# Performance work log

Hardware: AMD Instinct MI355X
Metric: run time of the kernel (lower is better)

## Reference

```python
import jax, jax.numpy as jnp
import numpy as np

B, S, D = 8, 1024, 1024
H = 16
HD = D // H  # 64
FF = 4 * D   # 4096
EPS = 1e-5


def layer_norm(x, g, b):
    mu = jnp.mean(x, axis=-1, keepdims=True)
    var = jnp.mean(jnp.square(x - mu), axis=-1, keepdims=True)
    return (x - mu) * jax.lax.rsqrt(var + EPS) * g + b


def setup_inputs() -> dict:
    key = jax.random.key(0)
    ks = jax.random.split(key, 16)
    s_in = 1.0 / np.sqrt(D)
    s_ff = 1.0 / np.sqrt(FF)
    return {
        "x": jax.random.normal(ks[0], (B, S, D), jnp.float32),
        "ln1_g": jnp.ones((D,), jnp.float32),
        "ln1_b": jnp.zeros((D,), jnp.float32),
        "ln2_g": jnp.ones((D,), jnp.float32),
        "ln2_b": jnp.zeros((D,), jnp.float32),
        # per-head projections stacked on a leading head axis: [H, D, HD]
        "Wq": jax.random.uniform(ks[1], (H, D, HD), jnp.float32, -s_in, s_in),
        "bq": jax.random.uniform(ks[2], (H, HD), jnp.float32, -s_in, s_in),
        "Wk": jax.random.uniform(ks[3], (H, D, HD), jnp.float32, -s_in, s_in),
        "bk": jax.random.uniform(ks[4], (H, HD), jnp.float32, -s_in, s_in),
        "Wv": jax.random.uniform(ks[5], (H, D, HD), jnp.float32, -s_in, s_in),
        "bv": jax.random.uniform(ks[6], (H, HD), jnp.float32, -s_in, s_in),
        "Wo": jax.random.uniform(ks[7], (D, D), jnp.float32, -s_in, s_in),
        "bo": jax.random.uniform(ks[8], (D,), jnp.float32, -s_in, s_in),
        "W1": jax.random.uniform(ks[9], (D, FF), jnp.float32, -s_in, s_in),
        "b1": jax.random.uniform(ks[10], (FF,), jnp.float32, -s_in, s_in),
        "W2": jax.random.uniform(ks[11], (FF, D), jnp.float32, -s_ff, s_ff),
        "b2": jax.random.uniform(ks[12], (D,), jnp.float32, -s_ff, s_ff),
    }


def attention(h, Wq, bq, Wk, bk, Wv, bv, Wo, bo):
    # h: [B,S,D] -> q/k/v: [B,H,S,HD]
    q = jnp.einsum("bsd,hdk->bhsk", h, Wq) + bq[None, :, None, :]
    k = jnp.einsum("bsd,hdk->bhsk", h, Wk) + bk[None, :, None, :]
    v = jnp.einsum("bsd,hdk->bhsk", h, Wv) + bv[None, :, None, :]
    scores = jnp.einsum("bhsk,bhtk->bhst", q, k) / jnp.sqrt(jnp.float32(HD))
    w = jax.nn.softmax(scores, axis=-1)  # [B,H,S,S]
    o = jnp.einsum("bhst,bhtk->bhsk", w, v)
    # concat heads (head order matches torch.cat over per-head outputs)
    o = o.transpose(0, 2, 1, 3).reshape(h.shape[0], h.shape[1], D)
    return o @ Wo + bo


def reference(x, ln1_g, ln1_b, ln2_g, ln2_b, Wq, bq, Wk, bk, Wv, bv, Wo, bo, W1, b1, W2, b2):
    h = layer_norm(x, ln1_g, ln1_b)
    x = x + attention(h, Wq, bq, Wk, bk, Wv, bv, Wo, bo)
    h2 = layer_norm(x, ln2_g, ln2_b)
    ff = jax.nn.gelu(h2 @ W1 + b1, approximate=False) @ W2 + b2  # dropout in eval = identity
    return x + ff
```

## Files before the change

### kernel.cpp

```cpp
#include <hip/hip_runtime.h>
#include <hip/hip_bf16.h>
#include <math.h>

#define DMODEL 1024
#define NH     16
#define HD     64
#define FFDIM  4096
#define SEQ    1024
#define BATCH  8
#define ROWS   (BATCH * SEQ)

typedef __bf16 bf16x8 __attribute__((ext_vector_type(8)));
typedef __bf16 bf16x4 __attribute__((ext_vector_type(4)));
typedef float  f32x4  __attribute__((ext_vector_type(4)));

__device__ __forceinline__ unsigned short f2bf(float f) {
  unsigned int u = __builtin_bit_cast(unsigned int, f);
  u += 0x7fff + ((u >> 16) & 1);
  return (unsigned short)(u >> 16);
}

__device__ __forceinline__ void gload_lds16(const void* g, void* l) {
  __builtin_amdgcn_global_load_lds(
      (const __attribute__((address_space(1))) unsigned int*)g,
      (__attribute__((address_space(3))) unsigned int*)l, 16, 0, 0);
}

__device__ __forceinline__ bf16x8 tr_read8(const unsigned short* p) {
  bf16x4 lo, hi;
  const __attribute__((address_space(3))) unsigned short* p3 =
      (const __attribute__((address_space(3))) unsigned short*)p;
  asm volatile("ds_read_b64_tr_b16 %0, %2\n\t"
               "ds_read_b64_tr_b16 %1, %2 offset:128"
               : "=v"(lo), "=v"(hi)
               : "v"(p3));
  return __builtin_shufflevector(lo, hi, 0, 1, 2, 3, 4, 5, 6, 7);
}

__global__ __launch_bounds__(256) void ln_bf16_kernel(
    const float* __restrict__ x, const float* __restrict__ g,
    const float* __restrict__ bta, unsigned short* __restrict__ out) {
  int row = blockIdx.x;
  int tid = threadIdx.x;
  int wid = tid >> 6, lane = tid & 63;
  const float4 v = ((const float4*)(x + (size_t)row * DMODEL))[tid];
  float s = v.x + v.y + v.z + v.w;
#pragma unroll
  for (int off = 32; off >= 1; off >>= 1) s += __shfl_xor(s, off, 64);
  __shared__ float red[8];
  if (lane == 0) red[wid] = s;
  __syncthreads();
  float mu = (red[0] + red[1] + red[2] + red[3]) * (1.0f / DMODEL);
  float4 d;
  d.x = v.x - mu; d.y = v.y - mu; d.z = v.z - mu; d.w = v.w - mu;
  float sq = d.x * d.x + d.y * d.y + d.z * d.z + d.w * d.w;
#pragma unroll
  for (int off = 32; off >= 1; off >>= 1) sq += __shfl_xor(sq, off, 64);
  if (lane == 0) red[4 + wid] = sq;
  __syncthreads();
  float var = (red[4] + red[5] + red[6] + red[7]) * (1.0f / DMODEL);
  float rs = rsqrtf(var + 1e-5f);
  const float4 gg = ((const float4*)g)[tid];
  const float4 bb = ((const float4*)bta)[tid];
  ushort4 o;
  o.x = f2bf(d.x * rs * gg.x + bb.x);
  o.y = f2bf(d.y * rs * gg.y + bb.y);
  o.z = f2bf(d.z * rs * gg.z + bb.z);
  o.w = f2bf(d.w * rs * gg.w + bb.w);
  ((ushort4*)(out + (size_t)row * DMODEL))[tid] = o;
}

__global__ __launch_bounds__(256) void transpose_f2b_kernel(
    const float* __restrict__ in, unsigned short* __restrict__ out,
    int R, int C, long long ibs, long long obs) {
  __shared__ float tile[64][65];
  int b = blockIdx.z;
  int r0 = blockIdx.y * 64, c0 = blockIdx.x * 64;
  const float* ip = in + (size_t)b * ibs;
  unsigned short* op = out + (size_t)b * obs;
  int tid = threadIdx.x;
  int rl = tid >> 4, cl = (tid & 15) * 4;
#pragma unroll
  for (int it = 0; it < 4; ++it) {
    int r = it * 16 + rl;
    float4 v = *(const float4*)(ip + (size_t)(r0 + r) * C + c0 + cl);
    tile[r][cl] = v.x; tile[r][cl + 1] = v.y;
    tile[r][cl + 2] = v.z; tile[r][cl + 3] = v.w;
  }
  __syncthreads();
#pragma unroll
  for (int it = 0; it < 4; ++it) {
    int c = it * 16 + rl;
    ushort4 o;
    o.x = f2bf(tile[cl + 0][c]); o.y = f2bf(tile[cl + 1][c]);
    o.z = f2bf(tile[cl + 2][c]); o.w = f2bf(tile[cl + 3][c]);
    *(ushort4*)(op + (size_t)(c0 + c) * R + r0 + cl) = o;
  }
}

__global__ __launch_bounds__(256) void transpose_v_kernel(
    const unsigned short* __restrict__ V, unsigned short* __restrict__ Vt) {
  __shared__ unsigned short tile[64][68];
  int bh = blockIdx.y;
  int b = bh >> 4, h = bh & 15;
  int t0 = blockIdx.x * 64;
  int tid = threadIdx.x;
  int rl = tid >> 4, cl = (tid & 15) * 4;
  const unsigned short* ip = V + ((size_t)(b * SEQ + t0)) * DMODEL + h * HD;
#pragma unroll
  for (int it = 0; it < 4; ++it) {
    int t = it * 16 + rl;
    ushort4 v = *(const ushort4*)(ip + (size_t)t * DMODEL + cl);
    tile[t][cl] = v.x; tile[t][cl + 1] = v.y;
    tile[t][cl + 2] = v.z; tile[t][cl + 3] = v.w;
  }
  __syncthreads();
  unsigned short* op = Vt + ((size_t)bh * HD) * SEQ + t0;
#pragma unroll
  for (int it = 0; it < 4; ++it) {
    int d = it * 16 + rl;
    ushort4 o;
    o.x = tile[cl + 0][d]; o.y = tile[cl + 1][d];
    o.z = tile[cl + 2][d]; o.w = tile[cl + 3][d];
    *(ushort4*)(op + (size_t)d * SEQ + cl) = o;
  }
}

#define QSCALE 0.18033688f
template <int EPI>
__global__ __launch_bounds__(256, 2) void gemm_kernel(
    const unsigned short* __restrict__ A, const unsigned short* __restrict__ Bt,
    const float* __restrict__ bias, const float* __restrict__ resid,
    unsigned short* __restrict__ outb, float* __restrict__ outf,
    int M, int N, int K) {
  __shared__ __align__(16) unsigned short As[128 * 32];
  __shared__ __align__(16) unsigned short Bs[128 * 32];
  int tid = threadIdx.x;
  int wid = tid >> 6, lane = tid & 63;
  int wr = (wid >> 1) * 64, wc = (wid & 1) * 64;
  int by = blockIdx.y * 128, bx = blockIdx.x * 128;
  int l15 = lane & 15, l4 = lane >> 4;
  const f32x4 fz = {0.f, 0.f, 0.f, 0.f};
  f32x4 acc[4][4];
#pragma unroll
  for (int i = 0; i < 4; ++i)
#pragma unroll
    for (int j = 0; j < 4; ++j) acc[i][j] = fz;

  int srow = tid >> 2;
  int schunk = tid & 3;

  for (int k0 = 0; k0 < K; k0 += 32) {
    __syncthreads();
#pragma unroll
    for (int p = 0; p < 2; ++p) {
      int row = p * 64 + srow;
      int g = schunk ^ ((row >> 1) & 3);
      gload_lds16(A + (size_t)(by + row) * K + k0 + g * 8,
                  (char*)As + p * 4096 + tid * 16);
      gload_lds16(Bt + (size_t)(bx + row) * K + k0 + g * 8,
                  (char*)Bs + p * 4096 + tid * 16);
    }
    __syncthreads();
    bf16x8 af[4], bfr[4];
#pragma unroll
    for (int m = 0; m < 4; ++m) {
      int row = wr + m * 16 + l15;
      int phys = l4 ^ ((row >> 1) & 3);
      af[m] = *(const bf16x8*)((const char*)As + row * 64 + phys * 16);
    }
#pragma unroll
    for (int n = 0; n < 4; ++n) {
      int row = wc + n * 16 + l15;
      int phys = l4 ^ ((row >> 1) & 3);
      bfr[n] = *(const bf16x8*)((const char*)Bs + row * 64 + phys * 16);
    }
#pragma unroll
    for (int m = 0; m < 4; ++m)
#pragma unroll
      for (int n = 0; n < 4; ++n)
        acc[m][n] = __builtin_amdgcn_mfma_f32_16x16x32_bf16(af[m], bfr[n],
                                                            acc[m][n], 0, 0, 0);
  }
#pragma unroll
  for (int m = 0; m < 4; ++m) {
#pragma unroll
    for (int n = 0; n < 4; ++n) {
      int col = bx + wc + n * 16 + l15;
      float bn = bias[col];
#pragma unroll
      for (int j = 0; j < 4; ++j) {
        int row = by + wr + m * 16 + l4 * 4 + j;
        float v = acc[m][n][j] + bn;
        if (EPI == 0) {
          outb[(size_t)row * N + col] = f2bf(v);
        } else if (EPI == 1) {
          outf[(size_t)row * N + col] = v + resid[(size_t)row * N + col];
        } else if (EPI == 2) {
          float gel = 0.5f * v * (1.0f + erff(v * 0.70710678118f));
          outb[(size_t)row * N + col] = f2bf(gel);
        } else if (EPI == 3) {
          outf[(size_t)row * N + col] = v + resid[(size_t)row * N + col];
        } else {
          outb[(size_t)row * N + col] = f2bf(v * QSCALE);
        }
      }
    }
  }
}

__global__ __launch_bounds__(256, 3) void attn_kernel(
    const unsigned short* __restrict__ Q, const unsigned short* __restrict__ K,
    const unsigned short* __restrict__ Vt, unsigned short* __restrict__ O) {
  __shared__ __align__(16) unsigned short Ks[128 * 64];
  __shared__ __align__(16) unsigned short Vs[64 * 128];
  __shared__ __align__(16) unsigned short Ps[4][128 * 16];
  int tid = threadIdx.x, wid = tid >> 6, lane = tid & 63;
  int l15 = lane & 15, l4 = lane >> 4;
  int sid = blockIdx.x;
  int aid = (sid & 7) * 256 + (sid >> 3);
  int bh = aid >> 4, qb = aid & 15;
  int b = bh >> 4, h = bh & 15;
  int q0 = qb * 64 + wid * 16;
  const f32x4 fz = {0.f, 0.f, 0.f, 0.f};

  const unsigned short* Qbase = Q + ((size_t)(b * SEQ + q0)) * DMODEL + h * HD;
  bf16x8 qf[2];
#pragma unroll
  for (int kh = 0; kh < 2; ++kh)
    qf[kh] = *(const bf16x8*)(Qbase + (size_t)l15 * DMODEL + kh * 32 + l4 * 8);

  f32x4 o[4];
#pragma unroll
  for (int i = 0; i < 4; ++i) o[i] = fz;
  float mrun[4], lrun[4];
#pragma unroll
  for (int j = 0; j < 4; ++j) { mrun[j] = -1e30f; lrun[j] = 0.0f; }

  const unsigned short* Kb = K + (size_t)b * SEQ * DMODEL + h * HD;
  const unsigned short* Vb = Vt + (size_t)bh * HD * SEQ;
  unsigned short* pbase = &Ps[wid][0];
  int krow = tid >> 3, kchunk = tid & 7;
  int vrow = tid >> 4, vchunk = tid & 15;

  for (int t0 = 0; t0 < SEQ; t0 += 128) {
    __syncthreads();
#pragma unroll
    for (int p = 0; p < 4; ++p) {
      int kr = p * 32 + krow;
      int kg = kchunk ^ (kr & 7);
      gload_lds16(Kb + (size_t)(t0 + kr) * DMODEL + kg * 8,
                  (char*)Ks + p * 4096 + tid * 16);
      int vr = p * 16 + vrow;
      int vg = vchunk ^ (vr & 7);
      gload_lds16(Vb + (size_t)vr * SEQ + t0 + vg * 8,
                  (char*)Vs + p * 4096 + tid * 16);
    }
    __syncthreads();
    f32x4 s[8];
#pragma unroll
    for (int ts = 0; ts < 8; ++ts) {
      int row = ts * 16 + l15;
      bf16x8 k0f = *(const bf16x8*)((const char*)Ks + row * 128 + ((l4) ^ (row & 7)) * 16);
      bf16x8 k1f = *(const bf16x8*)((const char*)Ks + row * 128 + ((4 + l4) ^ (row & 7)) * 16);
      s[ts] = __builtin_amdgcn_mfma_f32_16x16x32_bf16(qf[0], k0f, fz, 0, 0, 0);
      s[ts] = __builtin_amdgcn_mfma_f32_16x16x32_bf16(qf[1], k1f, s[ts], 0, 0, 0);
    }
#pragma unroll
    for (int j = 0; j < 4; ++j) {
      float tm = fmaxf(fmaxf(fmaxf(s[0][j], s[1][j]), fmaxf(s[2][j], s[3][j])),
                       fmaxf(fmaxf(s[4][j], s[5][j]), fmaxf(s[6][j], s[7][j])));
#pragma unroll
      for (int off = 8; off >= 1; off >>= 1) tm = fmaxf(tm, __shfl_xor(tm, off, 16));
      float mnew = fmaxf(mrun[j], tm);
      float alpha = __builtin_amdgcn_exp2f(mrun[j] - mnew);
      float ps = 0.0f;
#pragma unroll
      for (int ts = 0; ts < 8; ++ts) {
        float p = __builtin_amdgcn_exp2f(s[ts][j] - mnew);
        s[ts][j] = p;
        ps += p;
      }
#pragma unroll
      for (int off = 8; off >= 1; off >>= 1) ps += __shfl_xor(ps, off, 16);
      lrun[j] = lrun[j] * alpha + ps;
      mrun[j] = mnew;
#pragma unroll
      for (int d = 0; d < 4; ++d) o[d][j] *= alpha;
    }
#pragma unroll
    for (int ts = 0; ts < 8; ++ts) {
      ushort4 pk;
      pk.x = f2bf(s[ts][0]); pk.y = f2bf(s[ts][1]);
      pk.z = f2bf(s[ts][2]); pk.w = f2bf(s[ts][3]);
      *(ushort4*)((char*)pbase + (ts * 16 + l15) * 32 + l4 * 8) = pk;
    }
    asm volatile("s_waitcnt lgkmcnt(0)" ::: "memory");
    __builtin_amdgcn_sched_barrier(0);
#pragma unroll
    for (int kp = 0; kp < 4; ++kp) {
      bf16x8 pf = tr_read8(pbase + (kp * 32 + l4 * 8) * 16 + l15);
      asm volatile("s_waitcnt lgkmcnt(0)" ::: "memory");
      __builtin_amdgcn_sched_barrier(0);
#pragma unroll
      for (int d = 0; d < 4; ++d) {
        int vr = d * 16 + l15;
        int vphys = (kp * 4 + l4) ^ (vr & 7);
        bf16x8 vf = *(const bf16x8*)((const char*)Vs + vr * 256 + vphys * 16);
        o[d] = __builtin_amdgcn_mfma_f32_16x16x32_bf16(pf, vf, o[d], 0, 0, 0);
      }
    }
  }
  unsigned short* Ob = O + ((size_t)(b * SEQ + q0)) * DMODEL + h * HD;
#pragma unroll
  for (int j = 0; j < 4; ++j) {
    float inv = 1.0f / lrun[j];
#pragma unroll
    for (int d = 0; d < 4; ++d) {
      int row = l4 * 4 + j;
      Ob[(size_t)row * DMODEL + d * 16 + l15] = f2bf(o[d][j] * inv);
    }
  }
}

extern "C" void kernel_launch(void* const* d_in, const int* in_sizes, int n_in,
                              void* d_out, int out_size, void* d_ws, size_t ws_size,
                              hipStream_t stream) {
  (void)in_sizes; (void)n_in; (void)out_size; (void)ws_size;
  const float* x    = (const float*)d_in[0];
  const float* ln1g = (const float*)d_in[1];
  const float* ln1b = (const float*)d_in[2];
  const float* ln2g = (const float*)d_in[3];
  const float* ln2b = (const float*)d_in[4];
  const float* Wq   = (const float*)d_in[5];
  const float* bq   = (const float*)d_in[6];
  const float* Wk   = (const float*)d_in[7];
  const float* bk   = (const float*)d_in[8];
  const float* Wv   = (const float*)d_in[9];
  const float* bv   = (const float*)d_in[10];
  const float* Wo   = (const float*)d_in[11];
  const float* bo   = (const float*)d_in[12];
  const float* W1   = (const float*)d_in[13];
  const float* b1   = (const float*)d_in[14];
  const float* W2   = (const float*)d_in[15];
  const float* b2   = (const float*)d_in[16];
  float* out = (float*)d_out;

  char* ws = (char*)d_ws;
  const size_t MB = 1u << 20;
  unsigned short* wqT = (unsigned short*)(ws + 0 * MB);
  unsigned short* wkT = (unsigned short*)(ws + 2 * MB);
  unsigned short* wvT = (unsigned short*)(ws + 4 * MB);
  unsigned short* woT = (unsigned short*)(ws + 6 * MB);
  unsigned short* w1T = (unsigned short*)(ws + 8 * MB);
  unsigned short* w2T = (unsigned short*)(ws + 16 * MB);
  unsigned short* hb  = (unsigned short*)(ws + 24 * MB);
  unsigned short* Qb  = (unsigned short*)(ws + 40 * MB);
  unsigned short* Kb  = (unsigned short*)(ws + 56 * MB);
  unsigned short* Vb  = (unsigned short*)(ws + 72 * MB);
  unsigned short* Vt  = (unsigned short*)(ws + 88 * MB);
  unsigned short* Ob  = Vb;
  unsigned short* ff1 = (unsigned short*)(ws + 40 * MB);

  transpose_f2b_kernel<<<dim3(1, 16, 16), 256, 0, stream>>>(Wq, wqT, 1024, 64,
                                                            65536LL, 65536LL);
  transpose_f2b_kernel<<<dim3(1, 16, 16), 256, 0, stream>>>(Wk, wkT, 1024, 64,
                                                            65536LL, 65536LL);
  transpose_f2b_kernel<<<dim3(1, 16, 16), 256, 0, stream>>>(Wv, wvT, 1024, 64,
                                                            65536LL, 65536LL);
  transpose_f2b_kernel<<<dim3(16, 16, 1), 256, 0, stream>>>(Wo, woT, 1024, 1024, 0, 0);
  transpose_f2b_kernel<<<dim3(64, 16, 1), 256, 0, stream>>>(W1, w1T, 1024, 4096, 0, 0);
  transpose_f2b_kernel<<<dim3(16, 64, 1), 256, 0, stream>>>(W2, w2T, 4096, 1024, 0, 0);

  ln_bf16_kernel<<<dim3(ROWS), 256, 0, stream>>>(x, ln1g, ln1b, hb);

  gemm_kernel<4><<<dim3(8, 64), 256, 0, stream>>>(hb, wqT, bq, nullptr, Qb, nullptr,
                                                  ROWS, DMODEL, DMODEL);
  gemm_kernel<0><<<dim3(8, 64), 256, 0, stream>>>(hb, wkT, bk, nullptr, Kb, nullptr,
                                                  ROWS, DMODEL, DMODEL);
  gemm_kernel<0><<<dim3(8, 64), 256, 0, stream>>>(hb, wvT, bv, nullptr, Vb, nullptr,
                                                  ROWS, DMODEL, DMODEL);

  transpose_v_kernel<<<dim3(16, 128), 256, 0, stream>>>(Vb, Vt);

  attn_kernel<<<dim3(2048), 256, 0, stream>>>(Qb, Kb, Vt, Ob);

  gemm_kernel<1><<<dim3(8, 64), 256, 0, stream>>>(Ob, woT, bo, x, nullptr, out,
                                                  ROWS, DMODEL, DMODEL);

  ln_bf16_kernel<<<dim3(ROWS), 256, 0, stream>>>(out, ln2g, ln2b, hb);

  gemm_kernel<2><<<dim3(32, 64), 256, 0, stream>>>(hb, w1T, b1, nullptr, ff1, nullptr,
                                                   ROWS, FFDIM, DMODEL);

  gemm_kernel<3><<<dim3(8, 64), 256, 0, stream>>>(ff1, w2T, b2, out, nullptr, out,
                                                  ROWS, DMODEL, FFDIM);
}
```

Baseline: 449.3 us.

## Replace GEMM with 8-wave double-buffered pipelined kernel and larger tiles

```diff
diff --git a/kernel.cpp b/kernel.cpp
--- a/kernel.cpp
+++ b/kernel.cpp
@@ -35,6 +35,21 @@
                : "=v"(lo), "=v"(hi)
                : "v"(p3));
   return __builtin_shufflevector(lo, hi, 0, 1, 2, 3, 4, 5, 6, 7);
+}
+
+template <int N>
+__device__ __forceinline__ void wait_vm_lgkm() {
+  if constexpr (N == 0)
+    asm volatile("s_waitcnt vmcnt(0) lgkmcnt(0)" ::: "memory");
+  else if constexpr (N == 2)
+    asm volatile("s_waitcnt vmcnt(2) lgkmcnt(0)" ::: "memory");
+  else
+    asm volatile("s_waitcnt vmcnt(4) lgkmcnt(0)" ::: "memory");
+  __builtin_amdgcn_sched_barrier(0);
+}
+__device__ __forceinline__ void wait_lgkm() {
+  asm volatile("s_waitcnt lgkmcnt(0)" ::: "memory");
+  __builtin_amdgcn_sched_barrier(0);
 }
 
 __global__ __launch_bounds__(256) void ln_bf16_kernel(
@@ -127,86 +142,200 @@
 }
 
 #define QSCALE 0.18033688f
-template <int EPI>
-__global__ __launch_bounds__(256, 2) void gemm_kernel(
+
+template <int BN, int EPI>
+__global__ __launch_bounds__(512, 2) void gemm8_kernel(
     const unsigned short* __restrict__ A, const unsigned short* __restrict__ Bt,
     const float* __restrict__ bias, const float* __restrict__ resid,
     unsigned short* __restrict__ outb, float* __restrict__ outf,
-    int M, int N, int K) {
-  __shared__ __align__(16) unsigned short As[128 * 32];
-  __shared__ __align__(16) unsigned short Bs[128 * 32];
-  int tid = threadIdx.x;
-  int wid = tid >> 6, lane = tid & 63;
-  int wr = (wid >> 1) * 64, wc = (wid & 1) * 64;
-  int by = blockIdx.y * 128, bx = blockIdx.x * 128;
-  int l15 = lane & 15, l4 = lane >> 4;
+    int M, int N, int K, int NX) {
+  constexpr int WAVE_N = BN / 4;
+  constexpr int NREP = BN / 64;
+  constexpr int BSZB = BN * 128;
+  constexpr int VMN = (BN == 256) ? 4 : 2;
+  __shared__ __align__(16) unsigned short As[2 * 256 * 64];
+  __shared__ __align__(16) unsigned short Bs[2 * BN * 64];
+
+  const int tid = threadIdx.x;
+  const int wid = tid >> 6, lane = tid & 63;
+  const int l15 = lane & 15, l4 = lane >> 4;
+  const int wm = wid >> 2, wn = wid & 3;
+
+  const int cpx = (int)gridDim.x >> 3;
+  const int swz = ((int)blockIdx.x & 7) * cpx + ((int)blockIdx.x >> 3);
+  const int by = swz / NX, bx = swz % NX;
+
+  const size_t KBY = (size_t)K * 2;
+
+  const int rlA0 = wid * 16 + (lane >> 3);
+  const int rlA1 = rlA0 + 8;
+  const char* gA0 = (const char*)A + (size_t)(by * 256 + rlA0) * KBY +
+                    (((lane & 7) ^ (rlA0 & 7)) << 4);
+  const char* gA1 = (const char*)A + (size_t)(by * 256 + rlA1) * KBY +
+                    (((lane & 7) ^ (rlA1 & 7)) << 4);
+  char* ldsA0 = (char*)As + wid * 2048 + lane * 16;
+  char* ldsA1 = ldsA0 + 1024;
+
+  const int rlB0 = (BN == 256) ? (wid * 16 + (lane >> 3)) : (wid * 8 + (lane >> 3));
+  const int rlB1 = rlB0 + 8;
+  const char* gB0 = (const char*)Bt + (size_t)(bx * BN + rlB0) * KBY +
+                    (((lane & 7) ^ (rlB0 & 7)) << 4);
+  const char* gB1 = (const char*)Bt + (size_t)(bx * BN + rlB1) * KBY +
+                    (((lane & 7) ^ (rlB1 & 7)) << 4);
+  char* ldsB0 = (char*)Bs + ((BN == 256) ? (wid * 2048) : (wid * 1024)) + lane * 16;
+  char* ldsB1 = ldsB0 + 1024;
+
+  const char* aRd0 = (const char*)As + (wm * 128 + l15) * 128 + ((l4 ^ (l15 & 7)) << 4);
+  const char* aRd1 = (const char*)As + (wm * 128 + l15) * 128 + (((4 + l4) ^ (l15 & 7)) << 4);
+  const char* bRd0 = (const char*)Bs + (wn * WAVE_N + l15) * 128 + ((l4 ^ (l15 & 7)) << 4);
+  const char* bRd1 = (const char*)Bs + (wn * WAVE_N + l15) * 128 + (((4 + l4) ^ (l15 & 7)) << 4);
+
+  f32x4 acc[8][NREP];
   const f32x4 fz = {0.f, 0.f, 0.f, 0.f};
-  f32x4 acc[4][4];
-#pragma unroll
-  for (int i = 0; i < 4; ++i)
-#pragma unroll
-    for (int j = 0; j < 4; ++j) acc[i][j] = fz;
-
-  int srow = tid >> 2;
-  int schunk = tid & 3;
-
-  for (int k0 = 0; k0 < K; k0 += 32) {
-    __syncthreads();
-#pragma unroll
-    for (int p = 0; p < 2; ++p) {
-      int row = p * 64 + srow;
-      int g = schunk ^ ((row >> 1) & 3);
-      gload_lds16(A + (size_t)(by + row) * K + k0 + g * 8,
-                  (char*)As + p * 4096 + tid * 16);
-      gload_lds16(Bt + (size_t)(bx + row) * K + k0 + g * 8,
-                  (char*)Bs + p * 4096 + tid * 16);
-    }
-    __syncthreads();
-    bf16x8 af[4], bfr[4];
-#pragma unroll
-    for (int m = 0; m < 4; ++m) {
-      int row = wr + m * 16 + l15;
-      int phys = l4 ^ ((row >> 1) & 3);
-      af[m] = *(const bf16x8*)((const char*)As + row * 64 + phys * 16);
-    }
-#pragma unroll
-    for (int n = 0; n < 4; ++n) {
-      int row = wc + n * 16 + l15;
-      int phys = l4 ^ ((row >> 1) & 3);
-      bfr[n] = *(const bf16x8*)((const char*)Bs + row * 64 + phys * 16);
-    }
-#pragma unroll
-    for (int m = 0; m < 4; ++m)
-#pragma unroll
-      for (int n = 0; n < 4; ++n)
-        acc[m][n] = __builtin_amdgcn_mfma_f32_16x16x32_bf16(af[m], bfr[n],
-                                                            acc[m][n], 0, 0, 0);
-  }
-#pragma unroll
-  for (int m = 0; m < 4; ++m) {
-#pragma unroll
-    for (int n = 0; n < 4; ++n) {
-      int col = bx + wc + n * 16 + l15;
+#pragma unroll
+  for (int i = 0; i < 8; ++i)
+#pragma unroll
+    for (int n = 0; n < NREP; ++n) acc[i][n] = fz;
+  bf16x8 af[2][2];
+  bf16x8 baf[NREP][2];
+
+#define STAGE_A(buf, h, kt)                                                    \
+  do {                                                                         \
+    gload_lds16(gA0 + (size_t)(h) * 128 * KBY + (size_t)(kt) * 128,            \
+                ldsA0 + (buf) * 32768 + (h) * 16384);                          \
+    gload_lds16(gA1 + (size_t)(h) * 128 * KBY + (size_t)(kt) * 128,            \
+                ldsA1 + (buf) * 32768 + (h) * 16384);                          \
+  } while (0)
+
+#define STAGE_B(buf, h, kt)                                                    \
+  do {                                                                         \
+    if constexpr (BN == 256) {                                                 \
+      gload_lds16(gB0 + (size_t)(h) * 128 * KBY + (size_t)(kt) * 128,          \
+                  ldsB0 + (buf) * BSZB + (h) * 16384);                         \
+      gload_lds16(gB1 + (size_t)(h) * 128 * KBY + (size_t)(kt) * 128,          \
+                  ldsB1 + (buf) * BSZB + (h) * 16384);                         \
+    } else {                                                                   \
+      gload_lds16(gB0 + (size_t)(h) * 64 * KBY + (size_t)(kt) * 128,           \
+                  ldsB0 + (buf) * BSZB + (h) * 8192);                          \
+    }                                                                          \
+  } while (0)
+
+#define READ_B(buf)                                                            \
+  do {                                                                         \
+    _Pragma("unroll") for (int ni = 0; ni < NREP; ++ni) {                      \
+      baf[ni][0] = *(const bf16x8*)(bRd0 + (buf) * BSZB + ni * 2048);          \
+      baf[ni][1] = *(const bf16x8*)(bRd1 + (buf) * BSZB + ni * 2048);          \
+    }                                                                          \
+  } while (0)
+
+#define READ_A(buf, q)                                                         \
+  do {                                                                         \
+    _Pragma("unroll") for (int m01 = 0; m01 < 2; ++m01) {                      \
+      af[m01][0] = *(const bf16x8*)(aRd0 + (buf) * 32768 + (q) * 4096 + m01 * 2048); \
+      af[m01][1] = *(const bf16x8*)(aRd1 + (buf) * 32768 + (q) * 4096 + m01 * 2048); \
+    }                                                                          \
+  } while (0)
+
+#define MFMA_Q(q)                                                              \
+  do {                                                                         \
+    __builtin_amdgcn_s_setprio(1);                                             \
+    _Pragma("unroll") for (int m01 = 0; m01 < 2; ++m01)                        \
+        _Pragma("unroll") for (int ni = 0; ni < NREP; ++ni)                    \
+            _Pragma("unroll") for (int kk = 0; kk < 2; ++kk)                   \
+                acc[(q) * 2 + m01][ni] =                                       \
+        __builtin_amdgcn_mfma_f32_16x16x32_bf16(af[m01][kk], baf[ni][kk],      \
+                                                acc[(q) * 2 + m01][ni], 0, 0, 0); \
+    __builtin_amdgcn_s_setprio(0);                                             \
+  } while (0)
+
+#define BAR __builtin_amdgcn_s_barrier()
+
+#define ITER(t0, LAST)                                                         \
+  do {                                                                         \
+                                                                      \
+    READ_B(0); READ_A(0, 0);                                                   \
+    STAGE_A(1, 0, (t0) + 1);                                                   \
+    BAR; wait_lgkm(); MFMA_Q(0); BAR;                                          \
+                                                                      \
+    READ_A(0, 1);                                                              \
+    STAGE_A(1, 1, (t0) + 1);                                                   \
+    if (!(LAST)) STAGE_B(0, 0, (t0) + 2);                                      \
+    BAR; wait_lgkm(); MFMA_Q(1); BAR;                                          \
+                                                                      \
+    READ_A(0, 2);                                                              \
+    if (!(LAST)) STAGE_B(0, 1, (t0) + 2);                                      \
+    BAR; wait_lgkm(); MFMA_Q(2); BAR;                                          \
+                                                                      \
+    READ_A(0, 3);                                                              \
+    BAR;                                                                       \
+    if (LAST) wait_vm_lgkm<0>(); else wait_vm_lgkm<VMN>();                     \
+    MFMA_Q(3); BAR;                                                            \
+                                                                      \
+    READ_B(1); READ_A(1, 0);                                                   \
+    if (!(LAST)) STAGE_A(0, 0, (t0) + 2);                                      \
+    BAR; wait_lgkm(); MFMA_Q(0); BAR;                                          \
+                                                                      \
+    READ_A(1, 1);                                                              \
+    if (!(LAST)) STAGE_A(0, 1, (t0) + 2);                                      \
+    BAR; wait_lgkm(); MFMA_Q(1); BAR;                                          \
+                                                                      \
+    READ_A(1, 2);                                                              \
+    if (!(LAST)) STAGE_B(1, 0, (t0) + 3);                                      \
+    BAR; wait_lgkm(); MFMA_Q(2); BAR;                                          \
+                                                                      \
+    READ_A(1, 3);                                                              \
+    if (!(LAST)) STAGE_B(1, 1, (t0) + 3);                                      \
+    BAR;                                                                       \
+    if (LAST) wait_lgkm(); else wait_vm_lgkm<VMN>();                           \
+    MFMA_Q(3); BAR;                                                            \
+  } while (0)
+
+  const int nt = K >> 6;
+  const int J = (nt >> 1) - 1;
+
+  STAGE_A(0, 0, 0);
+  STAGE_A(0, 1, 0);
+  STAGE_B(0, 0, 0);
+  STAGE_B(0, 1, 0);
+  STAGE_B(1, 0, 1);
+  STAGE_B(1, 1, 1);
+  wait_vm_lgkm<VMN>();
+  BAR;
+
+#pragma unroll 1
+  for (int j = 0; j < J; ++j) ITER(2 * j, 0);
+  ITER(2 * J, 1);
+
+#pragma unroll
+  for (int mi = 0; mi < 8; ++mi) {
+#pragma unroll
+    for (int ni = 0; ni < NREP; ++ni) {
+      int col = bx * BN + wn * WAVE_N + ni * 16 + l15;
       float bn = bias[col];
 #pragma unroll
-      for (int j = 0; j < 4; ++j) {
-        int row = by + wr + m * 16 + l4 * 4 + j;
-        float v = acc[m][n][j] + bn;
+      for (int jj = 0; jj < 4; ++jj) {
+        int row = by * 256 + wm * 128 + mi * 16 + l4 * 4 + jj;
+        float v = acc[mi][ni][jj] + bn;
         if (EPI == 0) {
           outb[(size_t)row * N + col] = f2bf(v);
-        } else if (EPI == 1) {
+        } else if (EPI == 1 || EPI == 3) {
           outf[(size_t)row * N + col] = v + resid[(size_t)row * N + col];
         } else if (EPI == 2) {
           float gel = 0.5f * v * (1.0f + erff(v * 0.70710678118f));
           outb[(size_t)row * N + col] = f2bf(gel);
-        } else if (EPI == 3) {
-          outf[(size_t)row * N + col] = v + resid[(size_t)row * N + col];
         } else {
           outb[(size_t)row * N + col] = f2bf(v * QSCALE);
         }
       }
     }
   }
+#undef STAGE_A
+#undef STAGE_B
+#undef READ_A
+#undef READ_B
+#undef MFMA_Q
+#undef BAR
+#undef ITER
 }
 
 __global__ __launch_bounds__(256, 3) void attn_kernel(
@@ -374,25 +503,25 @@
 
   ln_bf16_kernel<<<dim3(ROWS), 256, 0, stream>>>(x, ln1g, ln1b, hb);
 
-  gemm_kernel<4><<<dim3(8, 64), 256, 0, stream>>>(hb, wqT, bq, nullptr, Qb, nullptr,
-                                                  ROWS, DMODEL, DMODEL);
-  gemm_kernel<0><<<dim3(8, 64), 256, 0, stream>>>(hb, wkT, bk, nullptr, Kb, nullptr,
-                                                  ROWS, DMODEL, DMODEL);
-  gemm_kernel<0><<<dim3(8, 64), 256, 0, stream>>>(hb, wvT, bv, nullptr, Vb, nullptr,
-                                                  ROWS, DMODEL, DMODEL);
+  gemm8_kernel<128, 4><<<dim3(256), 512, 0, stream>>>(hb, wqT, bq, nullptr, Qb,
+                                                      nullptr, ROWS, DMODEL, DMODEL, 8);
+  gemm8_kernel<128, 0><<<dim3(256), 512, 0, stream>>>(hb, wkT, bk, nullptr, Kb,
+                                                      nullptr, ROWS, DMODEL, DMODEL, 8);
+  gemm8_kernel<128, 0><<<dim3(256), 512, 0, stream>>>(hb, wvT, bv, nullptr, Vb,
+                                                      nullptr, ROWS, DMODEL, DMODEL, 8);
 
   transpose_v_kernel<<<dim3(16, 128), 256, 0, stream>>>(Vb, Vt);
 
   attn_kernel<<<dim3(2048), 256, 0, stream>>>(Qb, Kb, Vt, Ob);
 
-  gemm_kernel<1><<<dim3(8, 64), 256, 0, stream>>>(Ob, woT, bo, x, nullptr, out,
-                                                  ROWS, DMODEL, DMODEL);
+  gemm8_kernel<128, 1><<<dim3(256), 512, 0, stream>>>(Ob, woT, bo, x, nullptr, out,
+                                                      ROWS, DMODEL, DMODEL, 8);
 
   ln_bf16_kernel<<<dim3(ROWS), 256, 0, stream>>>(out, ln2g, ln2b, hb);
 
-  gemm_kernel<2><<<dim3(32, 64), 256, 0, stream>>>(hb, w1T, b1, nullptr, ff1, nullptr,
-                                                   ROWS, FFDIM, DMODEL);
-
-  gemm_kernel<3><<<dim3(8, 64), 256, 0, stream>>>(ff1, w2T, b2, out, nullptr, out,
-                                                  ROWS, DMODEL, FFDIM);
-}
+  gemm8_kernel<256, 2><<<dim3(512), 512, 0, stream>>>(hb, w1T, b1, nullptr, ff1,
+                                                      nullptr, ROWS, FFDIM, DMODEL, 16);
+
+  gemm8_kernel<128, 3><<<dim3(256), 512, 0, stream>>>(ff1, w2T, b2, out, nullptr, out,
+                                                      ROWS, DMODEL, FFDIM, 8);
+}
```

Result: faster. 411.1 us (-8.5%).

## Double-buffer GEMM with BK=64, 512-thread blocks, XCD swizzle, fused QKV launch

Applied to the files above, without the earlier changes.

```diff
diff --git a/kernel.cpp b/kernel.cpp
--- a/kernel.cpp
+++ b/kernel.cpp
@@ -127,82 +127,133 @@
 }
 
 #define QSCALE 0.18033688f
+
 template <int EPI>
-__global__ __launch_bounds__(256, 2) void gemm_kernel(
+__global__ __launch_bounds__(512, 4) void gemmdb_kernel(
     const unsigned short* __restrict__ A, const unsigned short* __restrict__ Bt,
-    const float* __restrict__ bias, const float* __restrict__ resid,
-    unsigned short* __restrict__ outb, float* __restrict__ outf,
-    int M, int N, int K) {
-  __shared__ __align__(16) unsigned short As[128 * 32];
-  __shared__ __align__(16) unsigned short Bs[128 * 32];
-  int tid = threadIdx.x;
-  int wid = tid >> 6, lane = tid & 63;
-  int wr = (wid >> 1) * 64, wc = (wid & 1) * 64;
-  int by = blockIdx.y * 128, bx = blockIdx.x * 128;
-  int l15 = lane & 15, l4 = lane >> 4;
+    const float* __restrict__ bias, const float* __restrict__ bias2,
+    const float* __restrict__ bias3, const float* __restrict__ resid,
+    unsigned short* __restrict__ outb, unsigned short* __restrict__ outb2,
+    unsigned short* __restrict__ outb3, float* __restrict__ outf,
+    int M, int N, int K, int NX) {
+  __shared__ __align__(16) unsigned short As[2 * 128 * 64];
+  __shared__ __align__(16) unsigned short Bs[2 * 128 * 64];
+
+  const int tid = threadIdx.x;
+  const int wid = tid >> 6, lane = tid & 63;
+  const int l15 = lane & 15, l4 = lane >> 4;
+  const int wm = wid >> 1, wn = wid & 1;
+
+  const int cpx = (int)gridDim.x >> 3;
+  const int swz = ((int)blockIdx.x & 7) * cpx + ((int)blockIdx.x >> 3);
+  const int by = swz / NX, bx = swz % NX;
+
+  const size_t KBY = (size_t)K * 2;
+
+  const int rS = tid >> 3;
+  const int cS = ((tid & 7) ^ (rS & 7)) << 4;
+  const char* gA = (const char*)A + (size_t)(by * 128 + rS) * KBY + cS;
+  const char* gB = (const char*)Bt + (size_t)(bx * 128 + rS) * KBY + cS;
+  char* sA = (char*)As + tid * 16;
+  char* sB = (char*)Bs + tid * 16;
+
+  const int rsw = (l4 ^ (l15 & 7)) << 4;
+  const char* aRd0 = (const char*)As + (wm * 32 + l15) * 128 + rsw;
+  const char* aRd1 = (const char*)As + (wm * 32 + l15) * 128 + (rsw ^ 64);
+  const char* bRd0 = (const char*)Bs + (wn * 64 + l15) * 128 + rsw;
+  const char* bRd1 = (const char*)Bs + (wn * 64 + l15) * 128 + (rsw ^ 64);
+
+  f32x4 acc[2][4];
   const f32x4 fz = {0.f, 0.f, 0.f, 0.f};
-  f32x4 acc[4][4];
-#pragma unroll
-  for (int i = 0; i < 4; ++i)
+#pragma unroll
+  for (int i = 0; i < 2; ++i)
 #pragma unroll
     for (int j = 0; j < 4; ++j) acc[i][j] = fz;
 
-  int srow = tid >> 2;
-  int schunk = tid & 3;
-
-  for (int k0 = 0; k0 < K; k0 += 32) {
-    __syncthreads();
-#pragma unroll
-    for (int p = 0; p < 2; ++p) {
-      int row = p * 64 + srow;
-      int g = schunk ^ ((row >> 1) & 3);
-      gload_lds16(A + (size_t)(by + row) * K + k0 + g * 8,
-                  (char*)As + p * 4096 + tid * 16);
-      gload_lds16(Bt + (size_t)(bx + row) * K + k0 + g * 8,
-                  (char*)Bs + p * 4096 + tid * 16);
-    }
-    __syncthreads();
-    bf16x8 af[4], bfr[4];
-#pragma unroll
-    for (int m = 0; m < 4; ++m) {
-      int row = wr + m * 16 + l15;
-      int phys = l4 ^ ((row >> 1) & 3);
-      af[m] = *(const bf16x8*)((const char*)As + row * 64 + phys * 16);
-    }
-#pragma unroll
-    for (int n = 0; n < 4; ++n) {
-      int row = wc + n * 16 + l15;
-      int phys = l4 ^ ((row >> 1) & 3);
-      bfr[n] = *(const bf16x8*)((const char*)Bs + row * 64 + phys * 16);
-    }
-#pragma unroll
-    for (int m = 0; m < 4; ++m)
-#pragma unroll
-      for (int n = 0; n < 4; ++n)
-        acc[m][n] = __builtin_amdgcn_mfma_f32_16x16x32_bf16(af[m], bfr[n],
-                                                            acc[m][n], 0, 0, 0);
-  }
-#pragma unroll
-  for (int m = 0; m < 4; ++m) {
-#pragma unroll
-    for (int n = 0; n < 4; ++n) {
-      int col = bx + wc + n * 16 + l15;
-      float bn = bias[col];
-#pragma unroll
-      for (int j = 0; j < 4; ++j) {
-        int row = by + wr + m * 16 + l4 * 4 + j;
-        float v = acc[m][n][j] + bn;
-        if (EPI == 0) {
-          outb[(size_t)row * N + col] = f2bf(v);
-        } else if (EPI == 1) {
-          outf[(size_t)row * N + col] = v + resid[(size_t)row * N + col];
-        } else if (EPI == 2) {
-          float gel = 0.5f * v * (1.0f + erff(v * 0.70710678118f));
-          outb[(size_t)row * N + col] = f2bf(gel);
-        } else if (EPI == 3) {
-          outf[(size_t)row * N + col] = v + resid[(size_t)row * N + col];
-        } else {
-          outb[(size_t)row * N + col] = f2bf(v * QSCALE);
+  const int nt = K >> 6;
+
+  gload_lds16(gA, sA);
+  gload_lds16(gA + 64 * KBY, sA + 8192);
+  gload_lds16(gB, sB);
+  gload_lds16(gB + 64 * KBY, sB + 8192);
+  asm volatile("s_waitcnt vmcnt(0)" ::: "memory");
+  __builtin_amdgcn_sched_barrier(0);
+  __builtin_amdgcn_s_barrier();
+  __builtin_amdgcn_sched_barrier(0);
+
+#pragma unroll 1
+  for (int t = 0; t < nt; ++t) {
+    const int cur = t & 1;
+    if (t + 1 < nt) {
+      const size_t ko = (size_t)(t + 1) << 7;
+      const int nb = (cur ^ 1) << 14;
+      gload_lds16(gA + ko, sA + nb);
+      gload_lds16(gA + 64 * KBY + ko, sA + nb + 8192);
+      gload_lds16(gB + ko, sB + nb);
+      gload_lds16(gB + 64 * KBY + ko, sB + nb + 8192);
+    }
+    const int off = cur << 14;
+#pragma unroll
+    for (int kk = 0; kk < 2; ++kk) {
+      const char* aR = (kk ? aRd1 : aRd0) + off;
+      const char* bR = (kk ? bRd1 : bRd0) + off;
+      bf16x8 afr[2], bfr[4];
+#pragma unroll
+      for (int ni = 0; ni < 4; ++ni) bfr[ni] = *(const bf16x8*)(bR + ni * 2048);
+#pragma unroll
+      for (int mi = 0; mi < 2; ++mi) afr[mi] = *(const bf16x8*)(aR + mi * 2048);
+      __builtin_amdgcn_s_setprio(1);
+#pragma unroll
+      for (int mi = 0; mi < 2; ++mi)
+#pragma unroll
+        for (int ni = 0; ni < 4; ++ni)
+          acc[mi][ni] = __builtin_amdgcn_mfma_f32_16x16x32_bf16(
+              afr[mi], bfr[ni], acc[mi][ni], 0, 0, 0);
+      __builtin_amdgcn_s_setprio(0);
+    }
+    asm volatile("s_waitcnt vmcnt(0)" ::: "memory");
+    __builtin_amdgcn_sched_barrier(0);
+    __builtin_amdgcn_s_barrier();
+    __builtin_amdgcn_sched_barrier(0);
+  }
+
+  if (EPI == 5) {
+    const int range = bx >> 3;
+    const float* bp = (range == 0) ? bias : (range == 1) ? bias2 : bias3;
+    unsigned short* op = (range == 0) ? outb : (range == 1) ? outb2 : outb3;
+    const float scale = (range == 0) ? QSCALE : 1.0f;
+#pragma unroll
+    for (int mi = 0; mi < 2; ++mi) {
+#pragma unroll
+      for (int ni = 0; ni < 4; ++ni) {
+        int colL = (bx & 7) * 128 + wn * 64 + ni * 16 + l15;
+        float bn = bp[colL];
+#pragma unroll
+        for (int jj = 0; jj < 4; ++jj) {
+          int row = by * 128 + wm * 32 + mi * 16 + l4 * 4 + jj;
+          op[(size_t)row * 1024 + colL] = f2bf((acc[mi][ni][jj] + bn) * scale);
+        }
+      }
+    }
+  } else {
+#pragma unroll
+    for (int mi = 0; mi < 2; ++mi) {
+#pragma unroll
+      for (int ni = 0; ni < 4; ++ni) {
+        int col = bx * 128 + wn * 64 + ni * 16 + l15;
+        float bn = bias[col];
+#pragma unroll
+        for (int jj = 0; jj < 4; ++jj) {
+          int row = by * 128 + wm * 32 + mi * 16 + l4 * 4 + jj;
+          float v = acc[mi][ni][jj] + bn;
+          if (EPI == 1 || EPI == 3) {
+            outf[(size_t)row * N + col] = v + resid[(size_t)row * N + col];
+          } else if (EPI == 2) {
+            float gel = 0.5f * v * (1.0f + erff(v * 0.70710678118f));
+            outb[(size_t)row * N + col] = f2bf(gel);
+          } else {
+            outb[(size_t)row * N + col] = f2bf(v);
+          }
         }
       }
     }
@@ -374,25 +425,24 @@
 
   ln_bf16_kernel<<<dim3(ROWS), 256, 0, stream>>>(x, ln1g, ln1b, hb);
 
-  gemm_kernel<4><<<dim3(8, 64), 256, 0, stream>>>(hb, wqT, bq, nullptr, Qb, nullptr,
-                                                  ROWS, DMODEL, DMODEL);
-  gemm_kernel<0><<<dim3(8, 64), 256, 0, stream>>>(hb, wkT, bk, nullptr, Kb, nullptr,
-                                                  ROWS, DMODEL, DMODEL);
-  gemm_kernel<0><<<dim3(8, 64), 256, 0, stream>>>(hb, wvT, bv, nullptr, Vb, nullptr,
-                                                  ROWS, DMODEL, DMODEL);
+  gemmdb_kernel<5><<<dim3(1536), 512, 0, stream>>>(
+      hb, wqT, bq, bk, bv, nullptr, Qb, Kb, Vb, nullptr, ROWS, 1024, DMODEL, 24);
 
   transpose_v_kernel<<<dim3(16, 128), 256, 0, stream>>>(Vb, Vt);
 
   attn_kernel<<<dim3(2048), 256, 0, stream>>>(Qb, Kb, Vt, Ob);
 
-  gemm_kernel<1><<<dim3(8, 64), 256, 0, stream>>>(Ob, woT, bo, x, nullptr, out,
-                                                  ROWS, DMODEL, DMODEL);
+  gemmdb_kernel<1><<<dim3(512), 512, 0, stream>>>(
+      Ob, woT, bo, nullptr, nullptr, x, nullptr, nullptr, nullptr, out,
+      ROWS, DMODEL, DMODEL, 8);
 
   ln_bf16_kernel<<<dim3(ROWS), 256, 0, stream>>>(out, ln2g, ln2b, hb);
 
-  gemm_kernel<2><<<dim3(32, 64), 256, 0, stream>>>(hb, w1T, b1, nullptr, ff1, nullptr,
-                                                   ROWS, FFDIM, DMODEL);
-
-  gemm_kernel<3><<<dim3(8, 64), 256, 0, stream>>>(ff1, w2T, b2, out, nullptr, out,
-                                                  ROWS, DMODEL, FFDIM);
-}
+  gemmdb_kernel<2><<<dim3(2048), 512, 0, stream>>>(
+      hb, w1T, b1, nullptr, nullptr, nullptr, ff1, nullptr, nullptr, nullptr,
+      ROWS, FFDIM, DMODEL, 32);
+
+  gemmdb_kernel<3><<<dim3(512), 512, 0, stream>>>(
+      ff1, w2T, b2, nullptr, nullptr, out, nullptr, nullptr, nullptr, out,
+      ROWS, DMODEL, FFDIM, 8);
+}
```

Result: faster. 403.6 us (-10.2%).
